# Optimization experiments

Hardware: AMD Instinct MI355X
Metric: run time of the kernel (lower is better)

Reference implementation:

```python
import jax, jax.numpy as jnp
import numpy as np

B, R, N, E, DIN, DOUT = 2, 2, 50000, 500000, 128, 128


def setup_inputs() -> dict:
    key = jax.random.key(0)
    k_x, k_src, k_dst, k_val, k_w = jax.random.split(key, 5)
    x = jax.random.normal(k_x, (B, N, DIN), dtype=jnp.float32)
    edge_src = jax.random.randint(k_src, (B, R, E), 0, N, dtype=jnp.int32)
    edge_dst = jax.random.randint(k_dst, (B, R, E), 0, N, dtype=jnp.int32)
    edge_val = jax.random.uniform(k_val, (B, R, E), dtype=jnp.float32)
    # Glorot-uniform init as in init_weight: range = sqrt(6/(fan_in+fan_out))
    init_range = float(np.sqrt(6.0 / (DIN + DOUT)))
    weights = jax.random.uniform(k_w, (R, DIN, DOUT), minval=-init_range,
                                 maxval=init_range, dtype=jnp.float32)
    bias = jnp.zeros((DOUT,), dtype=jnp.float32)
    return {"x": x, "edge_val": edge_val, "weights": weights, "bias": bias,
            "edge_src": edge_src, "edge_dst": edge_dst}


def reference(x, edge_val, weights, bias, edge_src, edge_dst):
    # Dense feature transform per relation: pre_sup = x @ W_r  -> [B, R, N, DOUT]
    pre = jnp.einsum('bnd,rde->brne', x, weights)
    bi = jnp.arange(B)[:, None, None]   # [B,1,1]
    ri = jnp.arange(R)[None, :, None]   # [1,R,1]
    # Sparse adjacency matmul A_r @ pre_sup:
    # out[dst] += A[dst, src] * pre_sup[src]  (edge list form)
    msgs = edge_val[..., None] * pre[bi, ri, edge_src]          # [B,R,E,DOUT]
    agg = jnp.zeros((B, R, N, DOUT), dtype=pre.dtype)
    agg = agg.at[bi, ri, edge_dst].add(msgs)                    # scatter-add
    # Sum across relations (tf.add_n), add bias, relu activation
    out = agg.sum(axis=1) + bias                                # [B,N,DOUT]
    return jax.nn.relu(out)
```

## Files before the change

kernel.cpp:

```cpp
#include <hip/hip_runtime.h>

#define BB 2
#define RR 2
#define NN 50000
#define EE 500000
#define DD 128
#define NSLOT 4
#define BSH 6
#define BSZ 64
#define NB 782
#define FT 8192
#define FBLK 62
#define SCAP 2048
#define DSTR 50048

#define A_PRE  0u
#define A_REC  12800000u
#define A_CNT  20800000u
#define A_OFS  20812544u
#define A_CUR  20825088u
#define A_DOF  20837632u
#define A_WT   21638400u

#define B_PRE  0u
#define B_REC  25600000u
#define B_CNT  33600000u
#define B_OFS  33612544u
#define B_CUR  33625088u
#define B_DOF  33637632u
#define B_WT   34438400u
#define B_TOTAL 34503936u

typedef __attribute__((ext_vector_type(8))) short bf16x8;
typedef __attribute__((ext_vector_type(4))) float f32x4;

__device__ __forceinline__ unsigned short f2bf(float f) {
    unsigned int u = __float_as_uint(f);
    u += 0x7fffu + ((u >> 16) & 1u);
    return (unsigned short)(u >> 16);
}

__device__ __forceinline__ bf16x8 pack8(float4 a, float4 b) {
    bf16x8 r;
    r[0] = (short)f2bf(a.x); r[1] = (short)f2bf(a.y);
    r[2] = (short)f2bf(a.z); r[3] = (short)f2bf(a.w);
    r[4] = (short)f2bf(b.x); r[5] = (short)f2bf(b.y);
    r[6] = (short)f2bf(b.z); r[7] = (short)f2bf(b.w);
    return r;
}

__global__ __launch_bounds__(256) void wprep_kernel(
    const float* __restrict__ w, unsigned short* __restrict__ wt)
{
    int idx = blockIdx.x * 256 + threadIdx.x;
    if (idx >= RR * DD * DD) return;
    int r = idx >> 14;
    int k = (idx >> 7) & (DD - 1);
    int n = idx & (DD - 1);
    wt[((size_t)r * DD + n) * DD + k] = f2bf(w[idx]);
}

template <int RST>
__global__ __launch_bounds__(256) void gemm_mfma_kernel(
    const float* __restrict__ x,
    const unsigned short* __restrict__ wt,
    unsigned short* __restrict__ pre)
{
    const int tid = threadIdx.x;
    const int w = tid >> 6, lane = tid & 63;
    const int wr = w >> 1, wc = w & 1;
    const int lq = lane >> 4, lr = lane & 15;
    const int row0 = blockIdx.x * 128;

    f32x4 acc[4][4] = {};

    #pragma unroll
    for (int ks = 0; ks < 4; ++ks) {
        const int k0 = ks * 32 + lq * 8;
        bf16x8 a[4], b[4];
        #pragma unroll
        for (int mi = 0; mi < 4; ++mi) {
            int row = row0 + wr * 64 + mi * 16 + lr;
            float4 v0 = make_float4(0.f, 0.f, 0.f, 0.f);
            float4 v1 = make_float4(0.f, 0.f, 0.f, 0.f);
            if (row < NN) {
                const float* p = x + (size_t)row * DD + k0;
                v0 = *(const float4*)p;
                v1 = *(const float4*)(p + 4);
            }
            a[mi] = pack8(v0, v1);
        }
        #pragma unroll
        for (int ni = 0; ni < 4; ++ni) {
            int n = wc * 64 + ni * 16 + lr;
            b[ni] = *(const bf16x8*)(wt + (size_t)n * DD + k0);
        }
        #pragma unroll
        for (int mi = 0; mi < 4; ++mi)
            #pragma unroll
            for (int ni = 0; ni < 4; ++ni)
                acc[mi][ni] = __builtin_amdgcn_mfma_f32_16x16x32_bf16(
                    a[mi], b[ni], acc[mi][ni], 0, 0, 0);
    }

    #pragma unroll
    for (int mi = 0; mi < 4; ++mi) {
        #pragma unroll
        for (int q = 0; q < 4; ++q) {
            int row = row0 + wr * 64 + mi * 16 + lq * 4 + q;
            if (row < NN) {
                #pragma unroll
                for (int ni = 0; ni < 4; ++ni) {
                    int col = wc * 64 + ni * 16 + lr;
                    pre[(size_t)row * RST + col] = f2bf(acc[mi][ni][q]);
                }
            }
        }
    }
}

__global__ __launch_bounds__(512) void gemm_mfma_dual_kernel(
    const float* __restrict__ x,
    const unsigned short* __restrict__ wt,
    unsigned short* __restrict__ pre)
{
    const int tid = threadIdx.x;
    const int w = tid >> 6, lane = tid & 63;
    const int wr = w >> 2, wc = w & 3;
    const int lq = lane >> 4, lr = lane & 15;
    const int row0 = blockIdx.x * 128;

    f32x4 acc[4][4] = {};

    #pragma unroll
    for (int ks = 0; ks < 4; ++ks) {
        const int k0 = ks * 32 + lq * 8;
        bf16x8 a[4], b[4];
        #pragma unroll
        for (int mi = 0; mi < 4; ++mi) {
            int row = row0 + wr * 64 + mi * 16 + lr;
            float4 v0 = make_float4(0.f, 0.f, 0.f, 0.f);
            float4 v1 = make_float4(0.f, 0.f, 0.f, 0.f);
            if (row < NN) {
                const float* p = x + (size_t)row * DD + k0;
                v0 = *(const float4*)p;
                v1 = *(const float4*)(p + 4);
            }
            a[mi] = pack8(v0, v1);
        }
        #pragma unroll
        for (int ni = 0; ni < 4; ++ni) {
            int n = wc * 64 + ni * 16 + lr;
            b[ni] = *(const bf16x8*)(wt + (size_t)n * DD + k0);
        }
        #pragma unroll
        for (int mi = 0; mi < 4; ++mi)
            #pragma unroll
            for (int ni = 0; ni < 4; ++ni)
                acc[mi][ni] = __builtin_amdgcn_mfma_f32_16x16x32_bf16(
                    a[mi], b[ni], acc[mi][ni], 0, 0, 0);
    }

    #pragma unroll
    for (int mi = 0; mi < 4; ++mi) {
        #pragma unroll
        for (int q = 0; q < 4; ++q) {
            int row = row0 + wr * 64 + mi * 16 + lq * 4 + q;
            if (row < NN) {
                #pragma unroll
                for (int ni = 0; ni < 4; ++ni) {
                    int col = wc * 64 + ni * 16 + lr;
                    pre[(size_t)row * (2 * DD) + col] = f2bf(acc[mi][ni][q]);
                }
            }
        }
    }
}

__global__ __launch_bounds__(256) void hist_kernel(
    const int* __restrict__ edst, int* __restrict__ counts)
{
    __shared__ int h[NB];
    for (int i = threadIdx.x; i < NB; i += 256) h[i] = 0;
    __syncthreads();
    const int slot = blockIdx.y;
    const int* ed = edst + (size_t)slot * EE;
    for (int e = blockIdx.x * 256 + threadIdx.x; e < EE; e += 128 * 256)
        atomicAdd(&h[ed[e] >> BSH], 1);
    __syncthreads();
    int* c = counts + slot * NB;
    for (int i = threadIdx.x; i < NB; i += 256) {
        int v = h[i];
        if (v) atomicAdd(&c[i], v);
    }
}

__global__ __launch_bounds__(1024) void scan_kernel(
    const int* __restrict__ counts, int* __restrict__ offsets,
    int* __restrict__ cursor)
{
    __shared__ int s[1024];
    const int slot = blockIdx.x;
    int v = (threadIdx.x < NB) ? counts[slot * NB + threadIdx.x] : 0;
    s[threadIdx.x] = v;
    for (int o = 1; o < 1024; o <<= 1) {
        __syncthreads();
        int t = (threadIdx.x >= o) ? s[threadIdx.x - o] : 0;
        __syncthreads();
        s[threadIdx.x] += t;
    }
    __syncthreads();
    if (threadIdx.x < NB) {
        int incl = s[threadIdx.x];
        offsets[slot * 784 + threadIdx.x + 1] = incl;
        cursor[slot * NB + threadIdx.x] = incl - v;
    }
    if (threadIdx.x == 0) offsets[slot * 784] = 0;
}

__global__ __launch_bounds__(1024) void fill_kernel(
    const int* __restrict__ esrc, const int* __restrict__ edst,
    const float* __restrict__ ev, int* __restrict__ cursor,
    unsigned int* __restrict__ recs)
{
    __shared__ int lh[NB];
    __shared__ int lbase[NB];
    const int slot = blockIdx.y;
    const size_t eb = (size_t)slot * EE;
    const int e0 = blockIdx.x * FT;

    for (int i = threadIdx.x; i < NB; i += 1024) lh[i] = 0;
    __syncthreads();
    for (int t = 0; t < FT; t += 1024) {
        int e = e0 + t + threadIdx.x;
        if (e < EE) atomicAdd(&lh[edst[eb + e] >> BSH], 1);
    }
    __syncthreads();
    for (int i = threadIdx.x; i < NB; i += 1024) {
        int c = lh[i];
        lbase[i] = c ? atomicAdd(&cursor[slot * NB + i], c) : 0;
        lh[i] = 0;
    }
    __syncthreads();
    for (int t = 0; t < FT; t += 1024) {
        int e = e0 + t + threadIdx.x;
        if (e < EE) {
            int d = edst[eb + e];
            int bk = d >> BSH;
            unsigned vq = (unsigned)__builtin_rintf(ev[eb + e] * 1023.0f);
            unsigned rec = (unsigned)esrc[eb + e] |
                           ((unsigned)(d & (BSZ - 1)) << 16) | (vq << 22);
            int p = lbase[bk] + atomicAdd(&lh[bk], 1);
            recs[eb + p] = rec;
        }
    }
}

__global__ __launch_bounds__(256) void sort_kernel(
    unsigned int* __restrict__ recs, const int* __restrict__ offsets,
    int* __restrict__ dofs)
{
    __shared__ unsigned int lrec[SCAP];
    __shared__ int cnt[BSZ];
    __shared__ int cur[BSZ];
    const int bk = blockIdx.x, slot = blockIdx.y;
    unsigned int* rp = recs + (size_t)slot * EE;
    const int s = offsets[slot * 784 + bk], e = offsets[slot * 784 + bk + 1];
    const int n = e - s;

    for (int i = threadIdx.x; i < n; i += 256) lrec[i] = rp[s + i];
    if (threadIdx.x < BSZ) cnt[threadIdx.x] = 0;
    __syncthreads();
    for (int i = threadIdx.x; i < n; i += 256)
        atomicAdd(&cnt[(lrec[i] >> 16) & (BSZ - 1)], 1);
    __syncthreads();
    if (threadIdx.x < 64) {
        int v = cnt[threadIdx.x];
        int incl = v;
        #pragma unroll
        for (int o = 1; o < 64; o <<= 1) {
            int t = __shfl_up(incl, o, 64);
            if (threadIdx.x >= o) incl += t;
        }
        int excl = incl - v;
        cur[threadIdx.x] = excl;
        dofs[(size_t)slot * DSTR + bk * BSZ + threadIdx.x] = s + excl;
    }
    __syncthreads();
    for (int i = threadIdx.x; i < n; i += 256) {
        unsigned r = lrec[i];
        int p = atomicAdd(&cur[(r >> 16) & (BSZ - 1)], 1);
        rp[s + p] = r;
    }
}

#define DEQ (1.0f / 1023.0f)
#define LO16(u) __uint_as_float((u) << 16)
#define HI16(u) __uint_as_float((u) & 0xffff0000u)

template <int SH, int OFF>
__device__ __forceinline__ void gacc(const unsigned short* __restrict__ pre,
                                     const unsigned int* __restrict__ rp,
                                     unsigned i, unsigned e, unsigned lane2,
                                     float& acc0, float& acc1)
{
    const unsigned base = (unsigned)OFF + lane2;
    for (; i + 8 <= e; i += 8) {
        unsigned q[8], u[8];
        #pragma unroll
        for (int j = 0; j < 8; ++j) q[j] = rp[i + j];
        #pragma unroll
        for (int j = 0; j < 8; ++j)
            u[j] = *(const unsigned*)(pre + (((q[j] & 0xffffu) << SH) + base));
        #pragma unroll
        for (int j = 0; j < 8; ++j) {
            float s = (float)(q[j] >> 22) * DEQ;
            acc0 = fmaf(s, LO16(u[j]), acc0);
            acc1 = fmaf(s, HI16(u[j]), acc1);
        }
    }
    if (i + 4 <= e) {
        unsigned q[4], u[4];
        #pragma unroll
        for (int j = 0; j < 4; ++j) q[j] = rp[i + j];
        #pragma unroll
        for (int j = 0; j < 4; ++j)
            u[j] = *(const unsigned*)(pre + (((q[j] & 0xffffu) << SH) + base));
        #pragma unroll
        for (int j = 0; j < 4; ++j) {
            float s = (float)(q[j] >> 22) * DEQ;
            acc0 = fmaf(s, LO16(u[j]), acc0);
            acc1 = fmaf(s, HI16(u[j]), acc1);
        }
        i += 4;
    }
    if (i + 2 <= e) {
        unsigned q0 = rp[i], q1 = rp[i + 1];
        unsigned u0 = *(const unsigned*)(pre + (((q0 & 0xffffu) << SH) + base));
        unsigned u1 = *(const unsigned*)(pre + (((q1 & 0xffffu) << SH) + base));
        float s0 = (float)(q0 >> 22) * DEQ, s1 = (float)(q1 >> 22) * DEQ;
        acc0 = fmaf(s0, LO16(u0), acc0); acc1 = fmaf(s0, HI16(u0), acc1);
        acc0 = fmaf(s1, LO16(u1), acc0); acc1 = fmaf(s1, HI16(u1), acc1);
        i += 2;
    }
    if (i < e) {
        unsigned q0 = rp[i];
        unsigned u0 = *(const unsigned*)(pre + (((q0 & 0xffffu) << SH) + base));
        float s0 = (float)(q0 >> 22) * DEQ;
        acc0 = fmaf(s0, LO16(u0), acc0); acc1 = fmaf(s0, HI16(u0), acc1);
    }
}

template <int FINAL>
__global__ __launch_bounds__(256) void gather_kernel(
    const unsigned short* __restrict__ pre, const unsigned int* __restrict__ rp,
    const int* __restrict__ dofs, const float* __restrict__ bias,
    float* __restrict__ out)
{
    const int d = blockIdx.x * 4 + (threadIdx.x >> 6);
    const unsigned lane2 = (threadIdx.x & 63) * 2;
    const unsigned i = dofs[d], e = dofs[d + 1];

    float2* o = (float2*)(out + (size_t)d * DD + lane2);
    float2 pv;
    float b0, b1;
    if (FINAL) {
        pv = *o;
        b0 = bias[lane2]; b1 = bias[lane2 + 1];
    }

    float acc0 = 0.f, acc1 = 0.f;
    gacc<7, 0>(pre, rp, i, e, lane2, acc0, acc1);

    if (FINAL) {
        pv.x = fmaxf(pv.x + acc0 + b0, 0.f);
        pv.y = fmaxf(pv.y + acc1 + b1, 0.f);
        *o = pv;
    } else {
        *o = make_float2(acc0, acc1);
    }
}

__global__ __launch_bounds__(256) void gather_dual_kernel(
    const unsigned short* __restrict__ preb,
    const unsigned int* __restrict__ rp0, const unsigned int* __restrict__ rp1,
    const int* __restrict__ dofs0, const int* __restrict__ dofs1,
    const float* __restrict__ bias, float* __restrict__ out)
{
    const int d = blockIdx.x * 4 + (threadIdx.x >> 6);
    const unsigned lane2 = (threadIdx.x & 63) * 2;
    const unsigned i0 = dofs0[d], e0 = dofs0[d + 1];
    const unsigned i1 = dofs1[d], e1 = dofs1[d + 1];

    float acc0 = 0.f, acc1 = 0.f;
    gacc<8, 0>(preb, rp0, i0, e0, lane2, acc0, acc1);
    gacc<8, DD>(preb, rp1, i1, e1, lane2, acc0, acc1);

    float2 pv;
    pv.x = fmaxf(acc0 + bias[lane2], 0.f);
    pv.y = fmaxf(acc1 + bias[lane2 + 1], 0.f);
    *(float2*)(out + (size_t)d * DD + lane2) = pv;
}

extern "C" void kernel_launch(void* const* d_in, const int* in_sizes, int n_in,
                              void* d_out, int out_size, void* d_ws, size_t ws_size,
                              hipStream_t stream) {
    const float* x     = (const float*)d_in[0];
    const float* eval_ = (const float*)d_in[1];
    const float* w     = (const float*)d_in[2];
    const float* bias  = (const float*)d_in[3];
    const int*   esrc  = (const int*)d_in[4];
    const int*   edst  = (const int*)d_in[5];
    float* out = (float*)d_out;

    const bool useB = (ws_size >= (size_t)B_TOTAL);

    char* ws = (char*)d_ws;
    unsigned short* pre     = (unsigned short*)(ws + (useB ? B_PRE : A_PRE));
    unsigned int*   recs    = (unsigned int*)(ws + (useB ? B_REC : A_REC));
    int*            counts  = (int*)(ws + (useB ? B_CNT : A_CNT));
    int*            offsets = (int*)(ws + (useB ? B_OFS : A_OFS));
    int*            cursor  = (int*)(ws + (useB ? B_CUR : A_CUR));
    int*            dofs    = (int*)(ws + (useB ? B_DOF : A_DOF));
    unsigned short* wt      = (unsigned short*)(ws + (useB ? B_WT : A_WT));

    const dim3 blk(256);

    hipMemsetAsync(counts, 0, NSLOT * NB * sizeof(int), stream);
    wprep_kernel<<<(RR * DD * DD + 255) / 256, blk, 0, stream>>>(w, wt);

    hist_kernel<<<dim3(128, NSLOT), blk, 0, stream>>>(edst, counts);
    scan_kernel<<<dim3(NSLOT), dim3(1024), 0, stream>>>(counts, offsets, cursor);
    fill_kernel<<<dim3(FBLK, NSLOT), dim3(1024), 0, stream>>>(
        esrc, edst, eval_, cursor, recs);
    sort_kernel<<<dim3(NB, NSLOT), blk, 0, stream>>>(recs, offsets, dofs);

    const dim3 gemm_grid((NN + 127) / 128);
    const dim3 gath_grid(NN / 4);

    if (useB) {
        for (int b = 0; b < BB; ++b) {
            const int s0 = b * RR, s1 = b * RR + 1;
            gemm_mfma_dual_kernel<<<gemm_grid, dim3(512), 0, stream>>>(
                x + (size_t)b * NN * DD, wt, pre);
            gather_dual_kernel<<<gath_grid, blk, 0, stream>>>(
                pre, recs + (size_t)s0 * EE, recs + (size_t)s1 * EE,
                dofs + (size_t)s0 * DSTR, dofs + (size_t)s1 * DSTR,
                bias, out + (size_t)b * NN * DD);
        }
    } else {
        for (int b = 0; b < BB; ++b) {
            for (int r = 0; r < RR; ++r) {
                const int slot = b * RR + r;
                gemm_mfma_kernel<DD><<<gemm_grid, blk, 0, stream>>>(
                    x + (size_t)b * NN * DD, wt + (size_t)r * DD * DD, pre);
                if (r == 0)
                    gather_kernel<0><<<gath_grid, blk, 0, stream>>>(
                        pre, recs + (size_t)slot * EE, dofs + (size_t)slot * DSTR,
                        bias, out + (size_t)b * NN * DD);
                else
                    gather_kernel<1><<<gath_grid, blk, 0, stream>>>(
                        pre, recs + (size_t)slot * EE, dofs + (size_t)slot * DSTR,
                        bias, out + (size_t)b * NN * DD);
            }
        }
    }
}
```

Before: 191.4 us.

## Sort edges by source within each destination and gather in source-range passes

The sort kernel now also insertion-sorts each destination's edge list by source index in shared memory. The dual gather kernel then walks both relations in lockstep across eight passes over source-index ranges, so that at any moment the workgroups in flight touch a narrower window of the pre-transformed feature table and hit in cache more often. The cost is a serial per-lane insertion sort in the sort kernel and a one-edge-at-a-time gather loop with per-edge branches and dependent loads, replacing the previous eight-wide unrolled batches. The gacc tail was also simplified to a scalar loop.

```diff
diff --git a/kernel.cpp b/kernel.cpp
--- a/kernel.cpp
+++ b/kernel.cpp
@@ -13,6 +13,8 @@
 #define FBLK 62
 #define SCAP 2048
 #define DSTR 50048
+#define NPASS 8
+#define PRNG 6250
 
 #define A_PRE  0u
 #define A_REC  12800000u
@@ -261,8 +263,10 @@
     int* __restrict__ dofs)
 {
     __shared__ unsigned int lrec[SCAP];
+    __shared__ unsigned int srec[SCAP];
     __shared__ int cnt[BSZ];
     __shared__ int cur[BSZ];
+    __shared__ int sstart[BSZ];
     const int bk = blockIdx.x, slot = blockIdx.y;
     unsigned int* rp = recs + (size_t)slot * EE;
     const int s = offsets[slot * 784 + bk], e = offsets[slot * 784 + bk + 1];
@@ -284,14 +288,32 @@
         }
         int excl = incl - v;
         cur[threadIdx.x] = excl;
+        sstart[threadIdx.x] = excl;
         dofs[(size_t)slot * DSTR + bk * BSZ + threadIdx.x] = s + excl;
     }
     __syncthreads();
     for (int i = threadIdx.x; i < n; i += 256) {
         unsigned r = lrec[i];
         int p = atomicAdd(&cur[(r >> 16) & (BSZ - 1)], 1);
-        rp[s + p] = r;
-    }
+        srec[p] = r;
+    }
+    __syncthreads();
+    if (threadIdx.x < 64) {
+        const int a = sstart[threadIdx.x];
+        const int m = cnt[threadIdx.x];
+        for (int j = 1; j < m; ++j) {
+            unsigned key = srec[a + j];
+            unsigned ks = key & 0xffffu;
+            int k = j - 1;
+            while (k >= 0 && (srec[a + k] & 0xffffu) > ks) {
+                srec[a + k + 1] = srec[a + k];
+                --k;
+            }
+            srec[a + k + 1] = key;
+        }
+    }
+    __syncthreads();
+    for (int i = threadIdx.x; i < n; i += 256) rp[s + i] = srec[i];
 }
 
 #define DEQ (1.0f / 1023.0f)
@@ -319,31 +341,7 @@
             acc1 = fmaf(s, HI16(u[j]), acc1);
         }
     }
-    if (i + 4 <= e) {
-        unsigned q[4], u[4];
-        #pragma unroll
-        for (int j = 0; j < 4; ++j) q[j] = rp[i + j];
-        #pragma unroll
-        for (int j = 0; j < 4; ++j)
-            u[j] = *(const unsigned*)(pre + (((q[j] & 0xffffu) << SH) + base));
-        #pragma unroll
-        for (int j = 0; j < 4; ++j) {
-            float s = (float)(q[j] >> 22) * DEQ;
-            acc0 = fmaf(s, LO16(u[j]), acc0);
-            acc1 = fmaf(s, HI16(u[j]), acc1);
-        }
-        i += 4;
-    }
-    if (i + 2 <= e) {
-        unsigned q0 = rp[i], q1 = rp[i + 1];
-        unsigned u0 = *(const unsigned*)(pre + (((q0 & 0xffffu) << SH) + base));
-        unsigned u1 = *(const unsigned*)(pre + (((q1 & 0xffffu) << SH) + base));
-        float s0 = (float)(q0 >> 22) * DEQ, s1 = (float)(q1 >> 22) * DEQ;
-        acc0 = fmaf(s0, LO16(u0), acc0); acc1 = fmaf(s0, HI16(u0), acc1);
-        acc0 = fmaf(s1, LO16(u1), acc0); acc1 = fmaf(s1, HI16(u1), acc1);
-        i += 2;
-    }
-    if (i < e) {
+    for (; i < e; ++i) {
         unsigned q0 = rp[i];
         unsigned u0 = *(const unsigned*)(pre + (((q0 & 0xffffu) << SH) + base));
         float s0 = (float)(q0 >> 22) * DEQ;
@@ -389,12 +387,45 @@
 {
     const int d = blockIdx.x * 4 + (threadIdx.x >> 6);
     const unsigned lane2 = (threadIdx.x & 63) * 2;
-    const unsigned i0 = dofs0[d], e0 = dofs0[d + 1];
-    const unsigned i1 = dofs1[d], e1 = dofs1[d + 1];
+    unsigned i0 = dofs0[d];
+    const unsigned e0 = dofs0[d + 1];
+    unsigned i1 = dofs1[d];
+    const unsigned e1 = dofs1[d + 1];
 
     float acc0 = 0.f, acc1 = 0.f;
-    gacc<8, 0>(preb, rp0, i0, e0, lane2, acc0, acc1);
-    gacc<8, DD>(preb, rp1, i1, e1, lane2, acc0, acc1);
+    unsigned q0 = 0, q1 = 0;
+    bool v0 = i0 < e0, v1 = i1 < e1;
+    if (v0) q0 = rp0[i0];
+    if (v1) q1 = rp1[i1];
+
+    #pragma unroll 1
+    for (unsigned p = 1; p <= NPASS; ++p) {
+        const unsigned bound = p * PRNG;
+        bool r0 = v0 && (q0 & 0xffffu) < bound;
+        bool r1 = v1 && (q1 & 0xffffu) < bound;
+        while (r0 || r1) {
+            if (r0) {
+                unsigned u0 = *(const unsigned*)(preb + (((q0 & 0xffffu) << 8) + lane2));
+                float s0 = (float)(q0 >> 22) * DEQ;
+                ++i0;
+                v0 = i0 < e0;
+                if (v0) q0 = rp0[i0];
+                acc0 = fmaf(s0, LO16(u0), acc0);
+                acc1 = fmaf(s0, HI16(u0), acc1);
+            }
+            if (r1) {
+                unsigned u1 = *(const unsigned*)(preb + (((q1 & 0xffffu) << 8) + DD + lane2));
+                float s1 = (float)(q1 >> 22) * DEQ;
+                ++i1;
+                v1 = i1 < e1;
+                if (v1) q1 = rp1[i1];
+                acc0 = fmaf(s1, LO16(u1), acc0);
+                acc1 = fmaf(s1, HI16(u1), acc1);
+            }
+            r0 = v0 && (q0 & 0xffffu) < bound;
+            r1 = v1 && (q1 & 0xffffu) < bound;
+        }
+    }
 
     float2 pv;
     pv.x = fmaxf(acc0 + bias[lane2], 0.f);
```

Result: slower. 306.9 us (+60.4%).
